# Optimization experiments

Hardware: AMD Instinct MI355X
Metric: run time of the kernel (lower is better)

The kernel has to match this reference:

```python
import jax, jax.numpy as jnp
import numpy as np

EPS_DIST = 1e-10
BN_EPS = 1e-5
K = 3  # nsample / three_nn


def setup_inputs() -> dict:
    key = jax.random.key(0)
    ks = jax.random.split(key, 8)
    B, N, S, D1, D2 = 4, 8192, 2048, 128, 256
    C_in = D1 + D2  # 384
    H = 256
    inp = {
        "pos1": jax.random.normal(ks[0], (B, 3, N), dtype=jnp.float32),
        "pos2": jax.random.normal(ks[1], (B, 3, S), dtype=jnp.float32),
        "feature1": jax.random.normal(ks[2], (B, D1, N), dtype=jnp.float32),
        "feature2": jax.random.normal(ks[3], (B, D2, S), dtype=jnp.float32),
        # MLP layer 1: Conv1d(384->256, k=1) + BN
        "W1": jax.random.normal(ks[4], (H, C_in), dtype=jnp.float32) * (1.0 / np.sqrt(C_in)),
        "b1": jnp.zeros((H,), dtype=jnp.float32),
        "g1": jnp.ones((H,), dtype=jnp.float32),
        "be1": jnp.zeros((H,), dtype=jnp.float32),
        # MLP layer 2: Conv1d(256->256, k=1) + BN
        "W2": jax.random.normal(ks[5], (H, H), dtype=jnp.float32) * (1.0 / np.sqrt(H)),
        "b2": jnp.zeros((H,), dtype=jnp.float32),
        "g2": jnp.ones((H,), dtype=jnp.float32),
        "be2": jnp.zeros((H,), dtype=jnp.float32),
    }
    return inp


def _conv_bn_relu(x, W, b, gamma, beta):
    # x: [B, Cin, N]; 1x1 Conv1d == channel GEMM
    y = jnp.einsum("oc,bcn->bon", W, x) + b[None, :, None]
    # BatchNorm1d in training mode: batch statistics over (B, N)
    mean = jnp.mean(y, axis=(0, 2), keepdims=True)
    var = jnp.mean(jnp.square(y - mean), axis=(0, 2), keepdims=True)
    y = (y - mean) * jax.lax.rsqrt(var + BN_EPS)
    y = y * gamma[None, :, None] + beta[None, :, None]
    return jax.nn.relu(y)


def reference(pos1, pos2, feature1, feature2, W1, b1, g1, be1, W2, b2, g2, be2):
    # pos1: [B,3,N], pos2: [B,3,S], feature1: [B,D1,N], feature2: [B,D2,S]
    p1 = jnp.swapaxes(pos1, 1, 2)  # [B,N,3]
    p2 = jnp.swapaxes(pos2, 1, 2)  # [B,S,3]
    # three_nn: squared-distance 3-NN of each point in p1 among p2
    d2 = (jnp.sum(p1 * p1, -1)[:, :, None]
          + jnp.sum(p2 * p2, -1)[:, None, :]
          - 2.0 * jnp.einsum("bnc,bsc->bns", p1, p2))  # [B,N,S]
    neg_vals, idx = jax.lax.top_k(-d2, K)  # idx: [B,N,3]
    dists = jnp.maximum(-neg_vals, EPS_DIST)  # dists[dists<1e-10]=1e-10
    w = 1.0 / dists
    w = w / jnp.sum(w, -1, keepdims=True)  # [B,N,3]
    # grouping_operation: gather feature2 [B,D,S] by idx -> [B,D,N,3]
    grouped = jax.vmap(lambda f, i: f[:, i])(feature2, idx)
    interpolated = jnp.sum(grouped * w[:, None, :, :], axis=-1)  # [B,D2,N]
    feat = jnp.concatenate([interpolated, feature1], axis=1)  # [B,384,N]
    feat = _conv_bn_relu(feat, W1, b1, g1, be1)
    feat = _conv_bn_relu(feat, W2, b2, g2, be2)
    return feat  # [B,256,N]
```

## Files before the change

### kernel.cpp

```cpp
#include <hip/hip_runtime.h>
#include <hip/hip_bf16.h>
#include <cstdint>

typedef unsigned short u16;
typedef unsigned int u32;
typedef unsigned long long u64;
typedef __bf16 bf16x8 __attribute__((ext_vector_type(8)));
typedef float f32x4 __attribute__((ext_vector_type(4)));
typedef u16 u16x8 __attribute__((ext_vector_type(8)));

__device__ __forceinline__ u16 f2b(float f) {
    unsigned int u = __float_as_uint(f);
    u += 0x7fffu + ((u >> 16) & 1u);
    return (u16)(u >> 16);
}
__device__ __forceinline__ float b2f(u16 h) {
    return __uint_as_float(((unsigned int)h) << 16);
}
__device__ __forceinline__ void async_cp16(void* lds, const void* g) {
    __builtin_amdgcn_global_load_lds((const __attribute__((address_space(1))) void*)g,
                                     (__attribute__((address_space(3))) void*)lds, 16, 0, 0);
}
__device__ __forceinline__ u32 fmono(float f) {
    u32 u = __float_as_uint(f);
    return u ^ (((u32)((int)u >> 31)) | 0x80000000u);
}
__device__ __forceinline__ u64 shfl_xor_u64(u64 v, int mask) {
    u32 lo = (u32)v, hi = (u32)(v >> 32);
    lo = (u32)__shfl_xor((int)lo, mask);
    hi = (u32)__shfl_xor((int)hi, mask);
    return ((u64)hi << 32) | lo;
}
__device__ __forceinline__ void ins3(u64 k, u64& k0, u64& k1, u64& k2) {
    bool c0 = k > k0, c1 = k > k1, c2 = k > k2;
    k2 = c1 ? k1 : (c2 ? k : k2);
    k1 = c0 ? k0 : (c1 ? k : k1);
    k0 = c0 ? k : k0;
}
__device__ __forceinline__ int pkix(int i) { return i + (i >> 6); }

#define NB_NN  512
#define NB_CVT 160
#define NB_T2  512
#define NB_T1  1024

__global__ __launch_bounds__(256, 4) void prep_kernel(const float* __restrict__ w1,
                                                      const float* __restrict__ w2,
                                                      u16* __restrict__ wb,
                                                      const float* __restrict__ feature2,
                                                      u16* __restrict__ f2t,
                                                      const float* __restrict__ feature1,
                                                      u16* __restrict__ f1t,
                                                      const float* __restrict__ pos1,
                                                      const float* __restrict__ pos2,
                                                      int* __restrict__ idx_out,
                                                      float* __restrict__ w_out) {
    __shared__ __align__(16) char smem[22784];
    int bi = blockIdx.x;
    int tid = threadIdx.x;

    if (bi >= NB_NN) {
        int ci = bi - NB_NN;
        if (ci < NB_CVT) {
            int i = ci * 256 + tid;
            if (i < 40960) {
                const float* src = (i < 24576) ? w1 : w2;
                int k = (i < 24576) ? i : (i - 24576);
                float4 v = *(const float4*)&src[(size_t)k * 4];
                ushort4 o;
                o.x = f2b(v.x); o.y = f2b(v.y); o.z = f2b(v.z); o.w = f2b(v.w);
                *(ushort4*)&wb[(size_t)i * 4] = o;
            }
            return;
        }
        float (*t)[65] = (float (*)[65])smem;
        const float* in; u16* out; int C, S, s0, c0, b;
        if (ci < NB_CVT + NB_T2) {
            int lin = ci - NB_CVT;
            C = 256; S = 2048; in = feature2; out = f2t;
            s0 = (lin & 31) * 64; c0 = ((lin >> 5) & 3) * 64; b = lin >> 7;
        } else {
            int lin = ci - NB_CVT - NB_T2;
            C = 128; S = 8192; in = feature1; out = f1t;
            s0 = (lin & 127) * 64; c0 = ((lin >> 7) & 1) * 64; b = lin >> 8;
        }
        const float* ib = in + (size_t)b * C * S;
        u16* ob = out + (size_t)b * S * C;
        int col = tid & 63, r0 = tid >> 6;
#pragma unroll
        for (int p = 0; p < 16; ++p) {
            int c = p * 4 + r0;
            t[c][col] = ib[(size_t)(c0 + c) * S + s0 + col];
        }
        __syncthreads();
#pragma unroll
        for (int p = 0; p < 16; ++p) {
            int s = p * 4 + r0;
            ob[(size_t)(s0 + s) * C + c0 + col] = f2b(t[col][s]);
        }
        return;
    }

    float4* pk = (float4*)smem;
    u64* warr = (u64*)(smem + 16640);
    int j0 = bi * 64;
    int b = j0 >> 13;
    const float* p2 = pos2 + (size_t)b * 3 * 2048;
    int p = tid & 15, ck = tid >> 4;
    int wv = tid >> 6, lane = tid & 63;
    const float* p1 = pos1 + (size_t)b * 3 * 8192;
    float qx[4], qy[4], qz[4];
#pragma unroll
    for (int t = 0; t < 4; ++t) {
        int n = (j0 & 8191) + p + t * 16;
        qx[t] = p1[n]; qy[t] = p1[8192 + n]; qz[t] = p1[16384 + n];
    }
    u64 key[4][3];
#pragma unroll
    for (int t = 0; t < 4; ++t) { key[t][0] = 0; key[t][1] = 0; key[t][2] = 0; }

    for (int half = 0; half < 2; ++half) {
        int hbase = half * 1024;
        for (int i = tid; i < 1024; i += 256) {
            int s = hbase + i;
            float x = p2[s], y = p2[2048 + s], z = p2[4096 + s];
            pk[pkix(i)] = make_float4(x, y, z, -0.5f * (x * x + y * y + z * z));
        }
        __syncthreads();

        float g[4][3]; int id[4][3];
#pragma unroll
        for (int t = 0; t < 4; ++t) {
            g[t][0] = -3.4e38f; g[t][1] = -3.4e38f; g[t][2] = -3.4e38f;
            id[t][0] = 0; id[t][1] = 0; id[t][2] = 0;
        }
        int sb = ck * 64;
        const float4* pc = pk + pkix(sb);
#pragma unroll 2
        for (int it = 0; it < 64; ++it) {
            float4 cd = pc[it];
            int s = sb + it;
#pragma unroll
            for (int t = 0; t < 4; ++t) {
                float tv = fmaf(qx[t], cd.x, fmaf(qy[t], cd.y, fmaf(qz[t], cd.z, cd.w)));
                bool c0 = tv > g[t][0], c1 = tv > g[t][1], c2 = tv > g[t][2];
                g[t][2] = c1 ? g[t][1] : (c2 ? tv : g[t][2]);
                id[t][2] = c1 ? id[t][1] : (c2 ? s : id[t][2]);
                g[t][1] = c0 ? g[t][0] : (c1 ? tv : g[t][1]);
                id[t][1] = c0 ? id[t][0] : (c1 ? s : id[t][1]);
                g[t][0] = c0 ? tv : g[t][0];
                id[t][0] = c0 ? s : id[t][0];
            }
        }
        __syncthreads();

#pragma unroll
        for (int t = 0; t < 4; ++t) {
#pragma unroll
            for (int r = 0; r < 3; ++r)
                ins3(((u64)fmono(g[t][r]) << 32) | (u64)(2047 - (hbase + id[t][r])),
                     key[t][0], key[t][1], key[t][2]);
        }
    }

#pragma unroll
    for (int mask = 16; mask <= 32; mask <<= 1) {
#pragma unroll
        for (int t = 0; t < 4; ++t) {
            u64 m0 = shfl_xor_u64(key[t][0], mask);
            u64 m1 = shfl_xor_u64(key[t][1], mask);
            u64 m2 = shfl_xor_u64(key[t][2], mask);
            ins3(m0, key[t][0], key[t][1], key[t][2]);
            ins3(m1, key[t][0], key[t][1], key[t][2]);
            ins3(m2, key[t][0], key[t][1], key[t][2]);
        }
    }
    if (lane < 16) {
        u64* wr = &warr[(wv * 16 + p) * 12];
#pragma unroll
        for (int t = 0; t < 4; ++t) {
            wr[t * 3 + 0] = key[t][0]; wr[t * 3 + 1] = key[t][1]; wr[t * 3 + 2] = key[t][2];
        }
    }
    __syncthreads();
    if (tid < 64) {
        int pp = tid & 15, t = tid >> 4;
        const u64* w0 = &warr[pp * 12 + t * 3];
        u64 k0 = w0[0], k1 = w0[1], k2 = w0[2];
#pragma unroll
        for (int w = 1; w < 4; ++w) {
            const u64* wr = &warr[(w * 16 + pp) * 12 + t * 3];
            ins3(wr[0], k0, k1, k2);
            ins3(wr[1], k0, k1, k2);
            ins3(wr[2], k0, k1, k2);
        }
        int s0 = 2047 - (int)(k0 & 0xFFFFFFFFu);
        int s1 = 2047 - (int)(k1 & 0xFFFFFFFFu);
        int s2 = 2047 - (int)(k2 & 0xFFFFFFFFu);
        int j = j0 + pp + t * 16;
        int n = j & 8191;
        float x1 = p1[n], y1 = p1[8192 + n], z1 = p1[16384 + n];
        float n1 = x1 * x1 + y1 * y1 + z1 * z1;
        float X0 = p2[s0], Y0 = p2[2048 + s0], Z0 = p2[4096 + s0];
        float X1 = p2[s1], Y1v = p2[2048 + s1], Z1 = p2[4096 + s1];
        float X2 = p2[s2], Y2v = p2[2048 + s2], Z2 = p2[4096 + s2];
        float t0 = x1 * X0 + y1 * Y0 + z1 * Z0 - 0.5f * (X0 * X0 + Y0 * Y0 + Z0 * Z0);
        float t1 = x1 * X1 + y1 * Y1v + z1 * Z1 - 0.5f * (X1 * X1 + Y1v * Y1v + Z1 * Z1);
        float t2 = x1 * X2 + y1 * Y2v + z1 * Z2 - 0.5f * (X2 * X2 + Y2v * Y2v + Z2 * Z2);
        float d0 = fmaxf(fmaf(-2.f, t0, n1), 1e-10f);
        float d1 = fmaxf(fmaf(-2.f, t1, n1), 1e-10f);
        float d2 = fmaxf(fmaf(-2.f, t2, n1), 1e-10f);
        float w0v = 1.f / d0, w1v = 1.f / d1, w2v = 1.f / d2;
        float inv = 1.f / (w0v + w1v + w2v);
        idx_out[j * 3] = s0; idx_out[j * 3 + 1] = s1; idx_out[j * 3 + 2] = s2;
        w_out[j * 3] = w0v * inv; w_out[j * 3 + 1] = w1v * inv; w_out[j * 3 + 2] = w2v * inv;
    }
}

template <int KT, bool GATHER, bool FUSE>
__global__ __launch_bounds__(256, 2) void gemm_kernel(const u16* __restrict__ A1,
                                                      const u16* __restrict__ A2,
                                                      const u16* __restrict__ Bw,
                                                      const float* __restrict__ bias,
                                                      const int* __restrict__ idx,
                                                      const float* __restrict__ wgt,
                                                      const float2* __restrict__ bnt_in,
                                                      u16* __restrict__ Yb,
                                                      float* __restrict__ Pt) {
    __shared__ __align__(16) char smemA[36864];
    u16* Al = (u16*)smemA;
    u16* Bl = (u16*)(smemA + 16384);
    u16* T  = (u16*)smemA;
    float2* BNT = (float2*)(smemA + 34816);
    int tid = threadIdx.x;
    int lane = tid & 63, wv = tid >> 6;
    int j0 = blockIdx.x * 128, m0 = blockIdx.y * 128;
    int l15 = lane & 15, q = lane >> 4;
    int wj = (wv >> 1) * 64, wm = (wv & 1) * 64;
    f32x4 acc[4][4];
#pragma unroll
    for (int i = 0; i < 4; ++i)
#pragma unroll
        for (int jj = 0; jj < 4; ++jj) acc[i][jj] = (f32x4){0.f, 0.f, 0.f, 0.f};

    int rbase = wv * 32;
    int lrow = lane >> 3, lchunk = lane & 7;
    int schunk = lchunk ^ lrow;
    const u16* Bg = Bw + (size_t)m0 * KT;

    if (FUSE) {
        BNT[tid] = bnt_in[tid];
        __syncthreads();
    }

    const u16* grow0[4]; const u16* grow1[4]; const u16* grow2[4];
    float gw0[4], gw1[4], gw2[4];
    if (GATHER) {
#pragma unroll
        for (int qq = 0; qq < 4; ++qq) {
            int jl = rbase + qq * 8 + lrow;
            int j = j0 + jl;
            int bb = j >> 13;
            const u16* fb = A1 + (size_t)bb * 2048 * 256;
            grow0[qq] = fb + (size_t)idx[j * 3 + 0] * 256;
            grow1[qq] = fb + (size_t)idx[j * 3 + 1] * 256;
            grow2[qq] = fb + (size_t)idx[j * 3 + 2] * 256;
            gw0[qq] = wgt[j * 3 + 0]; gw1[qq] = wgt[j * 3 + 1]; gw2[qq] = wgt[j * 3 + 2];
        }
    }

    for (int k0 = 0; k0 < KT; k0 += 64) {
#pragma unroll
        for (int qq = 0; qq < 4; ++qq) {
            int row = rbase + qq * 8;
            async_cp16(&Bl[row * 64], Bg + (size_t)(row + lrow) * KT + k0 + schunk * 8);
        }
        if (GATHER && k0 < 256) {
            int c = k0 + lchunk * 8;
#pragma unroll
            for (int qq = 0; qq < 4; ++qq) {
                int row = rbase + qq * 8;
                u16x8 v0 = *(const u16x8*)(grow0[qq] + c);
                u16x8 v1 = *(const u16x8*)(grow1[qq] + c);
                u16x8 v2 = *(const u16x8*)(grow2[qq] + c);
                u16x8 o;
#pragma unroll
                for (int e = 0; e < 8; ++e)
                    o[e] = f2b(gw0[qq] * b2f(v0[e]) + gw1[qq] * b2f(v1[e]) + gw2[qq] * b2f(v2[e]));
                *(u16x8*)&Al[(row + lrow) * 64 + schunk * 8] = o;
            }
        } else if (FUSE) {
            int c = k0 + lchunk * 8;
            float2 bn[8];
#pragma unroll
            for (int e = 0; e < 8; ++e) bn[e] = BNT[c + e];
#pragma unroll
            for (int qq = 0; qq < 4; ++qq) {
                int row = rbase + qq * 8;
                u16x8 y = *(const u16x8*)&A1[(size_t)(j0 + row + lrow) * 256 + c];
                u16x8 o;
#pragma unroll
                for (int e = 0; e < 8; ++e)
                    o[e] = f2b(fmaxf(b2f(y[e]) * bn[e].x + bn[e].y, 0.f));
                *(u16x8*)&Al[(row + lrow) * 64 + schunk * 8] = o;
            }
        } else {
            const u16* src = A2 + (size_t)j0 * 128 + (k0 - 256);
#pragma unroll
            for (int qq = 0; qq < 4; ++qq) {
                int row = rbase + qq * 8;
                async_cp16(&Al[row * 64], src + (size_t)(row + lrow) * 128 + schunk * 8);
            }
        }
        __syncthreads();
#pragma unroll
        for (int ks = 0; ks < 2; ++ks) {
            bf16x8 af[4], bfr[4];
#pragma unroll
            for (int i = 0; i < 4; ++i) {
                int row = wj + i * 16 + l15;
                af[i] = *(const bf16x8*)&Al[row * 64 + ((ks * 4 + q) ^ (l15 & 7)) * 8];
            }
#pragma unroll
            for (int i = 0; i < 4; ++i) {
                int row = wm + i * 16 + l15;
                bfr[i] = *(const bf16x8*)&Bl[row * 64 + ((ks * 4 + q) ^ (l15 & 7)) * 8];
            }
#pragma unroll
            for (int i = 0; i < 4; ++i)
#pragma unroll
                for (int jj = 0; jj < 4; ++jj)
                    acc[i][jj] = __builtin_amdgcn_mfma_f32_16x16x32_bf16(af[i], bfr[jj],
                                                                         acc[i][jj], 0, 0, 0);
        }
        __syncthreads();
    }
#pragma unroll
    for (int jj = 0; jj < 4; ++jj) {
        int ml = wm + jj * 16 + l15;
        float bv = bias[m0 + ml];
        float s = 0.f, s2 = 0.f;
#pragma unroll
        for (int i = 0; i < 4; ++i) {
            int jl = wj + i * 16 + q * 4;
#pragma unroll
            for (int r = 0; r < 4; ++r) {
                float v = acc[i][jj][r] + bv;
                s += v; s2 += v * v;
                T[(jl + r) * 136 + ml] = f2b(v);
            }
        }
        s += __shfl_xor(s, 16); s += __shfl_xor(s, 32);
        s2 += __shfl_xor(s2, 16); s2 += __shfl_xor(s2, 32);
        if (q == 0) {
            size_t prow = (size_t)blockIdx.x * 2 + (wv >> 1);
            Pt[prow * 512 + (m0 + ml)] = s;
            Pt[prow * 512 + 256 + (m0 + ml)] = s2;
        }
    }
    __syncthreads();
#pragma unroll
    for (int it = 0; it < 8; ++it) {
        int jl = it * 16 + wv * 4 + q;
        u16x8 v = *(const u16x8*)&T[jl * 136 + l15 * 8];
        *(u16x8*)&Yb[(size_t)(j0 + jl) * 256 + m0 + l15 * 8] = v;
    }
}

__global__ __launch_bounds__(256) void reduce_kernel(const float* __restrict__ P,
                                                     const float* __restrict__ g,
                                                     const float* __restrict__ be,
                                                     float2* __restrict__ bnt) {
    __shared__ float ls[4][64], ls2[4][64];
    int tid = threadIdx.x;
    int ch = blockIdx.x * 64 + (tid & 63);
    int rg = tid >> 6;
    float s = 0.f, s2 = 0.f;
    for (int r = rg * 128; r < rg * 128 + 128; ++r) {
        s += P[(size_t)r * 512 + ch];
        s2 += P[(size_t)r * 512 + 256 + ch];
    }
    ls[rg][tid & 63] = s; ls2[rg][tid & 63] = s2;
    __syncthreads();
    if (tid < 64) {
        float fs = ls[0][tid] + ls[1][tid] + ls[2][tid] + ls[3][tid];
        float fs2 = ls2[0][tid] + ls2[1][tid] + ls2[2][tid] + ls2[3][tid];
        int c = blockIdx.x * 64 + tid;
        const float inv = 1.f / 32768.f;
        float mean = fs * inv;
        float var = fs2 * inv - mean * mean;
        float a = g[c] * rsqrtf(var + 1e-5f);
        bnt[c] = make_float2(a, be[c] - mean * a);
    }
}

__global__ __launch_bounds__(256) void final_out_kernel(const u16* __restrict__ Y2,
                                                        const float2* __restrict__ bnt,
                                                        float* __restrict__ out) {
    __shared__ float t[64][65];
    int j0 = blockIdx.x * 64, o0 = blockIdx.y * 64;
    int tid = threadIdx.x;
    int c4 = (tid & 15) * 4, rw = tid >> 4;
#pragma unroll
    for (int p = 0; p < 4; ++p) {
        int jl = p * 16 + rw;
        ushort4 v = *(const ushort4*)&Y2[(size_t)(j0 + jl) * 256 + o0 + c4];
        t[jl][c4] = b2f(v.x); t[jl][c4 + 1] = b2f(v.y);
        t[jl][c4 + 2] = b2f(v.z); t[jl][c4 + 3] = b2f(v.w);
    }
    __syncthreads();
    int b = j0 >> 13, n0 = j0 & 8191;
#pragma unroll
    for (int p = 0; p < 4; ++p) {
        int ol = p * 16 + rw;
        int o = o0 + ol;
        float2 bn = bnt[o];
        float a = bn.x, s = bn.y;
        float4 v;
        v.x = fmaxf(t[c4][ol] * a + s, 0.f);
        v.y = fmaxf(t[c4 + 1][ol] * a + s, 0.f);
        v.z = fmaxf(t[c4 + 2][ol] * a + s, 0.f);
        v.w = fmaxf(t[c4 + 3][ol] * a + s, 0.f);
        *(float4*)&out[(size_t)b * 2097152 + (size_t)o * 8192 + n0 + c4] = v;
    }
}

extern "C" void kernel_launch(void* const* d_in, const int* in_sizes, int n_in,
                              void* d_out, int out_size, void* d_ws, size_t ws_size,
                              hipStream_t stream) {
    const float* pos1 = (const float*)d_in[0];
    const float* pos2 = (const float*)d_in[1];
    const float* feature1 = (const float*)d_in[2];
    const float* feature2 = (const float*)d_in[3];
    const float* W1 = (const float*)d_in[4];
    const float* b1 = (const float*)d_in[5];
    const float* g1 = (const float*)d_in[6];
    const float* be1 = (const float*)d_in[7];
    const float* W2 = (const float*)d_in[8];
    const float* b2 = (const float*)d_in[9];
    const float* g2 = (const float*)d_in[10];
    const float* be2 = (const float*)d_in[11];

    char* ws = (char*)d_ws;
    int*    IDX   = (int*)(ws + 0);
    float*  WGT   = (float*)(ws + 393216);
    u16*    W1B   = (u16*)(ws + 786432);
    u16*    W2B   = (u16*)(ws + 983040);
    float2* BNT1G = (float2*)(ws + 1114112);
    float2* BNT2G = (float2*)(ws + 1116160);
    u16*    F2T   = (u16*)(ws + 1118208);
    u16*    F1T   = (u16*)(ws + 5312512);
    u16*    Y1    = (u16*)(ws + 13701120);
    u16*    Y2    = (u16*)(ws + 30478336);
    float*  P1    = (float*)(ws + 47255552);
    float*  P2    = (float*)(ws + 48304128);
    float*  OUT   = (float*)d_out;

    prep_kernel<<<NB_NN + NB_CVT + NB_T2 + NB_T1, 256, 0, stream>>>(
        W1, W2, W1B, feature2, F2T, feature1, F1T, pos1, pos2, IDX, WGT);
    gemm_kernel<384, true, false><<<dim3(256, 2), 256, 0, stream>>>(
        F2T, F1T, W1B, b1, IDX, WGT, nullptr, Y1, P1);
    reduce_kernel<<<4, 256, 0, stream>>>(P1, g1, be1, BNT1G);
    gemm_kernel<256, false, true><<<dim3(256, 2), 256, 0, stream>>>(
        Y1, nullptr, W2B, b2, nullptr, nullptr, BNT1G, Y2, P2);
    reduce_kernel<<<4, 256, 0, stream>>>(P2, g2, be2, BNT2G);
    final_out_kernel<<<dim3(512, 4), 256, 0, stream>>>(Y2, BNT2G, OUT);
}
```

Baseline: 188.9 us.

## Split interpolation gather into its own kernel and halve points per NN block

The three-neighbour gather and weighted sum move out of the first GEMM into a separate interp_kernel that writes a bf16 interpolated matrix, so the GEMM can load A tiles with async global-to-LDS copies. The three-NN part of prep_kernel now handles 32 query points per block instead of 64, with twice as many blocks, higher occupancy bounds and less shared memory. The cost is an extra launch plus a write and re-read of the interpolated buffer (aliased onto Y2's workspace), and more redundant pos2 staging across NN blocks.

```diff
diff --git a/kernel.cpp b/kernel.cpp
--- a/kernel.cpp
+++ b/kernel.cpp
@@ -39,12 +39,12 @@
 }
 __device__ __forceinline__ int pkix(int i) { return i + (i >> 6); }
 
-#define NB_NN  512
+#define NB_NN  1024
 #define NB_CVT 160
 #define NB_T2  512
 #define NB_T1  1024
 
-__global__ __launch_bounds__(256, 4) void prep_kernel(const float* __restrict__ w1,
+__global__ __launch_bounds__(256, 6) void prep_kernel(const float* __restrict__ w1,
                                                       const float* __restrict__ w2,
                                                       u16* __restrict__ wb,
                                                       const float* __restrict__ feature2,
@@ -55,7 +55,7 @@
                                                       const float* __restrict__ pos2,
                                                       int* __restrict__ idx_out,
                                                       float* __restrict__ w_out) {
-    __shared__ __align__(16) char smem[22784];
+    __shared__ __align__(16) char smem[19712];
     int bi = blockIdx.x;
     int tid = threadIdx.x;
 
@@ -103,21 +103,21 @@
 
     float4* pk = (float4*)smem;
     u64* warr = (u64*)(smem + 16640);
-    int j0 = bi * 64;
+    int j0 = bi * 32;
     int b = j0 >> 13;
     const float* p2 = pos2 + (size_t)b * 3 * 2048;
     int p = tid & 15, ck = tid >> 4;
     int wv = tid >> 6, lane = tid & 63;
     const float* p1 = pos1 + (size_t)b * 3 * 8192;
-    float qx[4], qy[4], qz[4];
-#pragma unroll
-    for (int t = 0; t < 4; ++t) {
+    float qx[2], qy[2], qz[2];
+#pragma unroll
+    for (int t = 0; t < 2; ++t) {
         int n = (j0 & 8191) + p + t * 16;
         qx[t] = p1[n]; qy[t] = p1[8192 + n]; qz[t] = p1[16384 + n];
     }
-    u64 key[4][3];
-#pragma unroll
-    for (int t = 0; t < 4; ++t) { key[t][0] = 0; key[t][1] = 0; key[t][2] = 0; }
+    u64 key[2][3];
+#pragma unroll
+    for (int t = 0; t < 2; ++t) { key[t][0] = 0; key[t][1] = 0; key[t][2] = 0; }
 
     for (int half = 0; half < 2; ++half) {
         int hbase = half * 1024;
@@ -128,9 +128,9 @@
         }
         __syncthreads();
 
-        float g[4][3]; int id[4][3];
-#pragma unroll
-        for (int t = 0; t < 4; ++t) {
+        float g[2][3]; int id[2][3];
+#pragma unroll
+        for (int t = 0; t < 2; ++t) {
             g[t][0] = -3.4e38f; g[t][1] = -3.4e38f; g[t][2] = -3.4e38f;
             id[t][0] = 0; id[t][1] = 0; id[t][2] = 0;
         }
@@ -141,7 +141,7 @@
             float4 cd = pc[it];
             int s = sb + it;
 #pragma unroll
-            for (int t = 0; t < 4; ++t) {
+            for (int t = 0; t < 2; ++t) {
                 float tv = fmaf(qx[t], cd.x, fmaf(qy[t], cd.y, fmaf(qz[t], cd.z, cd.w)));
                 bool c0 = tv > g[t][0], c1 = tv > g[t][1], c2 = tv > g[t][2];
                 g[t][2] = c1 ? g[t][1] : (c2 ? tv : g[t][2]);
@@ -155,7 +155,7 @@
         __syncthreads();
 
 #pragma unroll
-        for (int t = 0; t < 4; ++t) {
+        for (int t = 0; t < 2; ++t) {
 #pragma unroll
             for (int r = 0; r < 3; ++r)
                 ins3(((u64)fmono(g[t][r]) << 32) | (u64)(2047 - (hbase + id[t][r])),
@@ -166,7 +166,7 @@
 #pragma unroll
     for (int mask = 16; mask <= 32; mask <<= 1) {
 #pragma unroll
-        for (int t = 0; t < 4; ++t) {
+        for (int t = 0; t < 2; ++t) {
             u64 m0 = shfl_xor_u64(key[t][0], mask);
             u64 m1 = shfl_xor_u64(key[t][1], mask);
             u64 m2 = shfl_xor_u64(key[t][2], mask);
@@ -176,20 +176,20 @@
         }
     }
     if (lane < 16) {
-        u64* wr = &warr[(wv * 16 + p) * 12];
-#pragma unroll
-        for (int t = 0; t < 4; ++t) {
+        u64* wr = &warr[(wv * 16 + p) * 6];
+#pragma unroll
+        for (int t = 0; t < 2; ++t) {
             wr[t * 3 + 0] = key[t][0]; wr[t * 3 + 1] = key[t][1]; wr[t * 3 + 2] = key[t][2];
         }
     }
     __syncthreads();
-    if (tid < 64) {
+    if (tid < 32) {
         int pp = tid & 15, t = tid >> 4;
-        const u64* w0 = &warr[pp * 12 + t * 3];
+        const u64* w0 = &warr[pp * 6 + t * 3];
         u64 k0 = w0[0], k1 = w0[1], k2 = w0[2];
 #pragma unroll
         for (int w = 1; w < 4; ++w) {
-            const u64* wr = &warr[(w * 16 + pp) * 12 + t * 3];
+            const u64* wr = &warr[(w * 16 + pp) * 6 + t * 3];
             ins3(wr[0], k0, k1, k2);
             ins3(wr[1], k0, k1, k2);
             ins3(wr[2], k0, k1, k2);
@@ -217,13 +217,38 @@
     }
 }
 
-template <int KT, bool GATHER, bool FUSE>
+__global__ __launch_bounds__(256, 8) void interp_kernel(const u16* __restrict__ f2t,
+                                                        const int* __restrict__ idx,
+                                                        const float* __restrict__ wgt,
+                                                        u16* __restrict__ out) {
+    int tid = threadIdx.x;
+    int j = blockIdx.x * 16 + (tid >> 4);
+    int c0 = (tid & 15) * 16;
+    int b = j >> 13;
+    const u16* fb = f2t + (size_t)b * 2048 * 256;
+    const u16* r0 = fb + (size_t)idx[j * 3 + 0] * 256 + c0;
+    const u16* r1 = fb + (size_t)idx[j * 3 + 1] * 256 + c0;
+    const u16* r2 = fb + (size_t)idx[j * 3 + 2] * 256 + c0;
+    float w0 = wgt[j * 3 + 0], w1 = wgt[j * 3 + 1], w2 = wgt[j * 3 + 2];
+    u16* ob = out + (size_t)j * 256 + c0;
+#pragma unroll
+    for (int cc = 0; cc < 2; ++cc) {
+        u16x8 v0 = *(const u16x8*)(r0 + cc * 8);
+        u16x8 v1 = *(const u16x8*)(r1 + cc * 8);
+        u16x8 v2 = *(const u16x8*)(r2 + cc * 8);
+        u16x8 o;
+#pragma unroll
+        for (int e = 0; e < 8; ++e)
+            o[e] = f2b(w0 * b2f(v0[e]) + w1 * b2f(v1[e]) + w2 * b2f(v2[e]));
+        *(u16x8*)(ob + cc * 8) = o;
+    }
+}
+
+template <int KT, bool FUSE>
 __global__ __launch_bounds__(256, 2) void gemm_kernel(const u16* __restrict__ A1,
                                                       const u16* __restrict__ A2,
                                                       const u16* __restrict__ Bw,
                                                       const float* __restrict__ bias,
-                                                      const int* __restrict__ idx,
-                                                      const float* __restrict__ wgt,
                                                       const float2* __restrict__ bnt_in,
                                                       u16* __restrict__ Yb,
                                                       float* __restrict__ Pt) {
@@ -253,43 +278,13 @@
         __syncthreads();
     }
 
-    const u16* grow0[4]; const u16* grow1[4]; const u16* grow2[4];
-    float gw0[4], gw1[4], gw2[4];
-    if (GATHER) {
-#pragma unroll
-        for (int qq = 0; qq < 4; ++qq) {
-            int jl = rbase + qq * 8 + lrow;
-            int j = j0 + jl;
-            int bb = j >> 13;
-            const u16* fb = A1 + (size_t)bb * 2048 * 256;
-            grow0[qq] = fb + (size_t)idx[j * 3 + 0] * 256;
-            grow1[qq] = fb + (size_t)idx[j * 3 + 1] * 256;
-            grow2[qq] = fb + (size_t)idx[j * 3 + 2] * 256;
-            gw0[qq] = wgt[j * 3 + 0]; gw1[qq] = wgt[j * 3 + 1]; gw2[qq] = wgt[j * 3 + 2];
-        }
-    }
-
     for (int k0 = 0; k0 < KT; k0 += 64) {
 #pragma unroll
         for (int qq = 0; qq < 4; ++qq) {
             int row = rbase + qq * 8;
             async_cp16(&Bl[row * 64], Bg + (size_t)(row + lrow) * KT + k0 + schunk * 8);
         }
-        if (GATHER && k0 < 256) {
-            int c = k0 + lchunk * 8;
-#pragma unroll
-            for (int qq = 0; qq < 4; ++qq) {
-                int row = rbase + qq * 8;
-                u16x8 v0 = *(const u16x8*)(grow0[qq] + c);
-                u16x8 v1 = *(const u16x8*)(grow1[qq] + c);
-                u16x8 v2 = *(const u16x8*)(grow2[qq] + c);
-                u16x8 o;
-#pragma unroll
-                for (int e = 0; e < 8; ++e)
-                    o[e] = f2b(gw0[qq] * b2f(v0[e]) + gw1[qq] * b2f(v1[e]) + gw2[qq] * b2f(v2[e]));
-                *(u16x8*)&Al[(row + lrow) * 64 + schunk * 8] = o;
-            }
-        } else if (FUSE) {
+        if (FUSE) {
             int c = k0 + lchunk * 8;
             float2 bn[8];
 #pragma unroll
@@ -305,11 +300,13 @@
                 *(u16x8*)&Al[(row + lrow) * 64 + schunk * 8] = o;
             }
         } else {
-            const u16* src = A2 + (size_t)j0 * 128 + (k0 - 256);
+            const u16* src; int str;
+            if (k0 < 256) { src = A1 + (size_t)j0 * 256 + k0;         str = 256; }
+            else          { src = A2 + (size_t)j0 * 128 + (k0 - 256); str = 128; }
 #pragma unroll
             for (int qq = 0; qq < 4; ++qq) {
                 int row = rbase + qq * 8;
-                async_cp16(&Al[row * 64], src + (size_t)(row + lrow) * 128 + schunk * 8);
+                async_cp16(&Al[row * 64], src + (size_t)(row + lrow) * str + schunk * 8);
             }
         }
         __syncthreads();
@@ -452,17 +449,19 @@
     u16*    F1T   = (u16*)(ws + 5312512);
     u16*    Y1    = (u16*)(ws + 13701120);
     u16*    Y2    = (u16*)(ws + 30478336);
+    u16*    INTERP= (u16*)(ws + 30478336);
     float*  P1    = (float*)(ws + 47255552);
     float*  P2    = (float*)(ws + 48304128);
     float*  OUT   = (float*)d_out;
 
     prep_kernel<<<NB_NN + NB_CVT + NB_T2 + NB_T1, 256, 0, stream>>>(
         W1, W2, W1B, feature2, F2T, feature1, F1T, pos1, pos2, IDX, WGT);
-    gemm_kernel<384, true, false><<<dim3(256, 2), 256, 0, stream>>>(
-        F2T, F1T, W1B, b1, IDX, WGT, nullptr, Y1, P1);
+    interp_kernel<<<2048, 256, 0, stream>>>(F2T, IDX, WGT, INTERP);
+    gemm_kernel<384, false><<<dim3(256, 2), 256, 0, stream>>>(
+        INTERP, F1T, W1B, b1, nullptr, Y1, P1);
     reduce_kernel<<<4, 256, 0, stream>>>(P1, g1, be1, BNT1G);
-    gemm_kernel<256, false, true><<<dim3(256, 2), 256, 0, stream>>>(
-        Y1, nullptr, W2B, b2, nullptr, nullptr, BNT1G, Y2, P2);
+    gemm_kernel<256, true><<<dim3(256, 2), 256, 0, stream>>>(
+        Y1, nullptr, W2B, b2, BNT1G, Y2, P2);
     reduce_kernel<<<4, 256, 0, stream>>>(P2, g2, be2, BNT2G);
     final_out_kernel<<<dim3(512, 4), 256, 0, stream>>>(Y2, BNT2G, OUT);
 }
```

Measured after the change: 189.6 us. No clear change (+0.4%).
